# Kernel optimization log

Hardware: AMD Instinct MI355X
Metric: run time of the kernel (lower is better)

Reference implementation:

```python
import jax, jax.numpy as jnp
import numpy as np

HIDDEN = 1024
HEADS = 16
HEAD_DIM = 64
B, S = 2, 2048
SCALE = 1.0 / np.sqrt(HEAD_DIM)
NEG = -1e9


def setup_inputs() -> dict:
    key = jax.random.key(0)
    k1, k2, k3, k4, k5 = jax.random.split(key, 5)
    hidden_states = jax.random.normal(k1, (B, S, HIDDEN), dtype=jnp.float32)
    # causal additive mask, broadcast over heads: [B, 1, S, S]
    causal = jnp.where(jnp.tril(jnp.ones((S, S), dtype=bool)), 0.0, NEG).astype(jnp.float32)
    attention_mask = jnp.broadcast_to(causal[None, None], (B, 1, S, S))
    std = 1.0 / np.sqrt(HIDDEN)
    Wq = jax.random.normal(k2, (HIDDEN, HEADS * HEAD_DIM), dtype=jnp.float32) * std
    Wk = jax.random.normal(k3, (HIDDEN, HEADS * HEAD_DIM), dtype=jnp.float32) * std
    Wv = jax.random.normal(k4, (HIDDEN, HEADS * HEAD_DIM), dtype=jnp.float32) * std
    Wo = jax.random.normal(k5, (HEADS * HEAD_DIM, HIDDEN), dtype=jnp.float32) * std
    return {"hidden_states": hidden_states, "attention_mask": attention_mask,
            "Wq": Wq, "Wk": Wk, "Wv": Wv, "Wo": Wo}


def reference(hidden_states, attention_mask, Wq, Wk, Wv, Wo):
    b, s, _ = hidden_states.shape
    # projections (eval mode: dropouts are identity)
    q = (hidden_states @ Wq).reshape(b, s, HEADS, HEAD_DIM).transpose(0, 2, 1, 3)  # [B,H,S,D]
    k = (hidden_states @ Wk).reshape(b, s, HEADS, HEAD_DIM).transpose(0, 2, 1, 3)
    v = (hidden_states @ Wv).reshape(b, s, HEADS, HEAD_DIM).transpose(0, 2, 1, 3)
    scores = jnp.einsum('bhqd,bhkd->bhqk', q, k) * SCALE + attention_mask  # [B,H,S,S]
    probs = jax.nn.softmax(scores, axis=-1)
    out = jnp.einsum('bhqk,bhkd->bhqd', probs, v)  # [B,H,S,D]
    out = out.transpose(0, 2, 1, 3).reshape(b, s, HEADS * HEAD_DIM)
    return out @ Wo  # [B,S,HIDDEN]
```

## Files before the change

### kernel.cpp

```cpp
#include <hip/hip_runtime.h>

typedef unsigned short u16;
typedef unsigned int u32;
typedef __bf16 bf16x8 __attribute__((ext_vector_type(8)));
typedef float f32x4 __attribute__((ext_vector_type(4)));

#define MFMA(a, b, c) __builtin_amdgcn_mfma_f32_16x16x32_bf16(a, b, c, 0, 0, 0)

#define GLD16(gsrc, ldst)                                                          \
  __builtin_amdgcn_global_load_lds(                                                \
      (const __attribute__((address_space(1))) void*)(gsrc),                       \
      (__attribute__((address_space(3))) void*)(ldst), 16, 0, 0)

#if __has_builtin(__builtin_amdgcn_exp2f)
#define EXP2(x) __builtin_amdgcn_exp2f(x)
#else
#define EXP2(x) exp2f(x)
#endif

__device__ __forceinline__ u16 f2bf(float f) {
  return __builtin_bit_cast(u16, (__bf16)f);
}

__device__ __forceinline__ u32 pk2(float a, float b) {
  __bf16 x = (__bf16)a, y = (__bf16)b;
  return (u32)__builtin_bit_cast(u16, x) | ((u32)__builtin_bit_cast(u16, y) << 16);
}

__device__ __forceinline__ float bf2f(u16 u) {
  return __builtin_bit_cast(float, ((u32)u) << 16);
}

__global__ __launch_bounds__(256) void k_prep(
    const float* __restrict__ X, const float* __restrict__ Wq,
    const float* __restrict__ Wk, const float* __restrict__ Wv,
    const float* __restrict__ Wo, u16* __restrict__ Xb,
    u16* __restrict__ Wt, u16* __restrict__ Wot) {
  __shared__ u16 t[32][33];
  int bid = blockIdx.x;
  if (bid < 2048) {
    int i = bid * 256 + threadIdx.x;
    const float4* p = (const float4*)X + (size_t)i * 2;
    float4 a = p[0], b = p[1];
    uint4 o;
    o.x = pk2(a.x, a.y);
    o.y = pk2(a.z, a.w);
    o.z = pk2(b.x, b.y);
    o.w = pk2(b.z, b.w);
    *(uint4*)(Xb + (size_t)i * 8) = o;
    return;
  }
  bid -= 2048;
  const int k0 = (bid & 31) * 32, n0 = (bid >> 5) * 32;
  const int x = threadIdx.x & 31, y = threadIdx.x >> 5;
  const float* src = (n0 < 1024) ? Wq : (n0 < 2048) ? Wk : (n0 < 3072) ? Wv : Wo;
  const int ncol = n0 & 1023;
#pragma unroll
  for (int rr = 0; rr < 4; ++rr) {
    int kl = y + rr * 8;
    t[x][kl] = f2bf(src[(size_t)(k0 + kl) * 1024 + ncol + x]);
  }
  __syncthreads();
  u16* dst = (n0 < 3072) ? (Wt + (size_t)n0 * 1024) : (Wot + (size_t)(n0 - 3072) * 1024);
#pragma unroll
  for (int rr = 0; rr < 4; ++rr) {
    int nl = y + rr * 8;
    dst[(size_t)nl * 1024 + k0 + x] = t[nl][x];
  }
}


__global__ __launch_bounds__(256) void k_gemm_qkv(const u16* __restrict__ A_,
                                                  const u16* __restrict__ Bt,
                                                  u16* __restrict__ Q,
                                                  u16* __restrict__ K,
                                                  u16* __restrict__ Vt) {
  __shared__ __align__(16) u16 As[2][128 * 32];
  __shared__ __align__(16) u16 Bs[2][64 * 32];
  const int tid = threadIdx.x;
  const int w = tid >> 6, l = tid & 63;
  const int lr = l & 15, lg = l >> 4;
  const int lin = blockIdx.y * 48 + blockIdx.x;
  const int swz = (lin & 7) * 192 + (lin >> 3);
  const int tM = (swz / 48) * 128, tN = (swz % 48) * 64;
  const int bufsel = tN >> 10;

  const int srow = l >> 2;
  const int scol = (((l & 3) ^ ((l >> 3) & 3)) << 3);
  const u16* Ag = A_ + (size_t)(tM + srow) * 1024 + scol;
  const u16* Bg = Bt + (size_t)(tN + srow) * 1024 + scol;
  const int rs = (lr >> 1) & 3;

#define STAGE_QKV(buf, kk)                                                   \
  {                                                                          \
    GLD16(Ag + (size_t)(w * 16) * 1024 + (kk), &As[buf][(w * 16) * 32]);     \
    GLD16(Ag + (size_t)(64 + w * 16) * 1024 + (kk), &As[buf][(64 + w * 16) * 32]); \
    GLD16(Bg + (size_t)(w * 16) * 1024 + (kk), &Bs[buf][(w * 16) * 32]);     \
  }

  f32x4 acc[2][4] = {};
  STAGE_QKV(0, 0)
  __syncthreads();
  int cur = 0;

  if (bufsel < 2) {
    for (int t = 0; t < 32; ++t) {
      if (t < 31) STAGE_QKV(cur ^ 1, (t + 1) * 32)
      const u16* Ac = &As[cur][0];
      const u16* Bc = &Bs[cur][0];
      bf16x8 a[2], b[4];
#pragma unroll
      for (int m = 0; m < 2; ++m)
        a[m] = *(const bf16x8*)(Ac + (w * 32 + m * 16 + lr) * 32 + ((lg ^ rs) << 3));
#pragma unroll
      for (int n = 0; n < 4; ++n)
        b[n] = *(const bf16x8*)(Bc + (n * 16 + lr) * 32 + ((lg ^ rs) << 3));
#pragma unroll
      for (int m = 0; m < 2; ++m)
#pragma unroll
        for (int n = 0; n < 4; ++n) acc[m][n] = MFMA(b[n], a[m], acc[m][n]);
      __syncthreads();
      cur ^= 1;
    }
    u16* dst = bufsel ? K : Q;
    const float sc = bufsel ? 1.0f : 0.180336880111124f;
#pragma unroll
    for (int m = 0; m < 2; ++m) {
      int s = tM + w * 32 + m * 16 + lr;
      int b_ = s >> 11, sr2 = s & 2047;
#pragma unroll
      for (int n = 0; n < 4; ++n) {
        int c2 = (tN + n * 16 + lg * 4) & 1023;
        int h = c2 >> 6, d = c2 & 63;
        uint2 val;
        val.x = pk2(acc[m][n][0] * sc, acc[m][n][1] * sc);
        val.y = pk2(acc[m][n][2] * sc, acc[m][n][3] * sc);
        *(uint2*)(dst + ((size_t)(b_ * 16 + h) * 2048 + sr2) * 64 + d) = val;
      }
    }
  } else {
    for (int t = 0; t < 32; ++t) {
      if (t < 31) STAGE_QKV(cur ^ 1, (t + 1) * 32)
      const u16* Ac = &As[cur][0];
      const u16* Bc = &Bs[cur][0];
      bf16x8 a[2], b[4];
#pragma unroll
      for (int m = 0; m < 2; ++m)
        a[m] = *(const bf16x8*)(Ac + (w * 32 + m * 16 + lr) * 32 + ((lg ^ rs) << 3));
#pragma unroll
      for (int n = 0; n < 4; ++n)
        b[n] = *(const bf16x8*)(Bc + (n * 16 + lr) * 32 + ((lg ^ rs) << 3));
#pragma unroll
      for (int m = 0; m < 2; ++m)
#pragma unroll
        for (int n = 0; n < 4; ++n) acc[m][n] = MFMA(a[m], b[n], acc[m][n]);
      __syncthreads();
      cur ^= 1;
    }
#pragma unroll
    for (int m = 0; m < 2; ++m) {
      int r0 = tM + w * 32 + m * 16 + lg * 4;
      int b_ = r0 >> 11, s0 = r0 & 2047;
#pragma unroll
      for (int n = 0; n < 4; ++n) {
        int c2 = (tN + n * 16 + lr) & 1023;
        int h = c2 >> 6, d = c2 & 63;
        uint2 val;
        val.x = pk2(acc[m][n][0], acc[m][n][1]);
        val.y = pk2(acc[m][n][2], acc[m][n][3]);
        *(uint2*)(Vt + ((size_t)(b_ * 16 + h) * 64 + d) * 2048 + s0) = val;
      }
    }
  }
#undef STAGE_QKV
}

__global__ __launch_bounds__(256, 4) void k_attn(const u16* __restrict__ Q,
                                                 const u16* __restrict__ Kg,
                                                 const u16* __restrict__ Vtg,
                                                 u16* __restrict__ AO,
                                                 u16* __restrict__ PO,
                                                 float* __restrict__ ML) {
  __shared__ __align__(16) u16 Ks[2][64 * 64];
  __shared__ __align__(16) u16 Vs[2][64 * 64];
  __shared__ __align__(16) u16 Ps[4][16 * 64];
  const int tid = threadIdx.x;
  const int w = tid >> 6, l = tid & 63;
  const int lr = l & 15, lg = l >> 4;

  const int idx = blockIdx.x;
  const int bh = idx & 31;
  const int g = idx >> 5;
  int qt, c0;
  if (g < 16) { qt = 16 + g; c0 = 0; }
  else if (g < 32) { qt = 31 - (g - 16); c0 = 1; }
  else { qt = 15 - (g - 32); c0 = 0; }
  const int nkt = (qt < 16) ? (qt + 1) : (c0 == 0 ? 16 : qt - 15);
  const bool hasdiag = (qt < 16) || (c0 == 1);
  const int q0 = qt * 64;

  const u16* Qp = Q + (size_t)bh * 2048 * 64;
  const u16* Kp = Kg + (size_t)bh * 2048 * 64;
  const u16* Vp = Vtg + (size_t)bh * 64 * 2048;

  const int qrow = q0 + w * 16 + lr;
  bf16x8 qa0 = *(const bf16x8*)(Qp + (size_t)qrow * 64 + lg * 8);
  bf16x8 qa1 = *(const bf16x8*)(Qp + (size_t)qrow * 64 + 32 + lg * 8);

  f32x4 oacc[4] = {};
  float m_run = -1e30f, l_run = 0.f;

  const int srow = l >> 3;
  const int scol = ((l & 7) ^ srow) * 8;
  const int sw = (lr & 7) << 3;

  const u16* kptr = Kp + ((size_t)c0 * 1024 + srow) * 64 + scol;
  const u16* vptr = Vp + (size_t)srow * 2048 + c0 * 1024 + scol;

#pragma unroll
  for (int j = 0; j < 2; ++j) {
    int base = j * 32 + w * 8;
    GLD16(kptr + base * 64, &Ks[0][base * 64]);
    GLD16(vptr + (size_t)base * 2048, &Vs[0][base * 64]);
  }
  kptr += 4096;
  vptr += 64;
  __syncthreads();

  int cur = 0;

#define ATTN_TILE(DOPRE, DOMASK)                                                   \
  {                                                                                \
    if (DOPRE) {                                                                   \
      _Pragma("unroll") for (int j = 0; j < 2; ++j) {                              \
        int base = j * 32 + w * 8;                                                 \
        GLD16(kptr + base * 64, &Ks[cur ^ 1][base * 64]);                          \
        GLD16(vptr + (size_t)base * 2048, &Vs[cur ^ 1][base * 64]);                \
      }                                                                            \
      kptr += 4096;                                                                \
      vptr += 64;                                                                  \
    }                                                                              \
    f32x4 st[4];                                                                   \
    _Pragma("unroll") for (int n = 0; n < 4; ++n) {                                \
      const u16* kr = &Ks[cur][(n * 16 + lr) * 64];                                \
      bf16x8 kb0 = *(const bf16x8*)(kr + ((lg << 3) ^ sw));                        \
      bf16x8 kb1 = *(const bf16x8*)(kr + (((4 + lg) << 3) ^ sw));                  \
      f32x4 z = {0.f, 0.f, 0.f, 0.f};                                              \
      z = MFMA(kb0, qa0, z);                                                       \
      z = MFMA(kb1, qa1, z);                                                       \
      st[n] = z;                                                                   \
    }                                                                              \
    float mx = -1e30f;                                                             \
    _Pragma("unroll") for (int n = 0; n < 4; ++n)                                  \
        _Pragma("unroll") for (int j = 0; j < 4; ++j) {                            \
      float s = st[n][j];                                                          \
      if (DOMASK && (n * 16 + lg * 4 + j) > (w * 16 + lr)) s = -1e30f;             \
      st[n][j] = s;                                                                \
      mx = fmaxf(mx, s);                                                           \
    }                                                                              \
    mx = fmaxf(mx, __shfl_xor(mx, 16, 64));                                        \
    mx = fmaxf(mx, __shfl_xor(mx, 32, 64));                                        \
    const bool grow = __any(mx > m_run);                                           \
    float mnew = grow ? fmaxf(m_run, mx) : m_run;                                  \
    float rsum = 0.f;                                                              \
    _Pragma("unroll") for (int n = 0; n < 4; ++n)                                  \
        _Pragma("unroll") for (int j = 0; j < 4; ++j) {                            \
      float p = EXP2(st[n][j] - mnew);                                             \
      st[n][j] = p;                                                                \
      rsum += p;                                                                   \
    }                                                                              \
    rsum += __shfl_xor(rsum, 16, 64);                                              \
    rsum += __shfl_xor(rsum, 32, 64);                                              \
    if (grow) {                                                                    \
      float fsc = EXP2(m_run - mnew);                                              \
      l_run = l_run * fsc + rsum;                                                  \
      m_run = mnew;                                                                \
      _Pragma("unroll") for (int n = 0; n < 4; ++n)                                \
          _Pragma("unroll") for (int j = 0; j < 4; ++j) oacc[n][j] *= fsc;         \
    } else {                                                                       \
      l_run += rsum;                                                               \
    }                                                                              \
    u16* pb = &Ps[w][0];                                                           \
    _Pragma("unroll") for (int n = 0; n < 4; ++n) {                                \
      int slot = n * 2 + (lg >> 1);                                                \
      int off = lr * 64 + ((slot ^ (lr & 7)) << 3) + (lg & 1) * 4;                 \
      uint2 val;                                                                   \
      val.x = pk2(st[n][0], st[n][1]);                                             \
      val.y = pk2(st[n][2], st[n][3]);                                             \
      *(uint2*)(pb + off) = val;                                                   \
    }                                                                              \
    bf16x8 pa0 = *(const bf16x8*)(pb + lr * 64 + ((lg << 3) ^ sw));                \
    bf16x8 pa1 = *(const bf16x8*)(pb + lr * 64 + (((4 + lg) << 3) ^ sw));          \
    _Pragma("unroll") for (int n = 0; n < 4; ++n) {                                \
      const u16* vr = &Vs[cur][(n * 16 + lr) * 64];                                \
      bf16x8 vb0 = *(const bf16x8*)(vr + ((lg << 3) ^ sw));                        \
      bf16x8 vb1 = *(const bf16x8*)(vr + (((4 + lg) << 3) ^ sw));                  \
      oacc[n] = MFMA(vb0, pa0, oacc[n]);                                           \
      oacc[n] = MFMA(vb1, pa1, oacc[n]);                                           \
    }                                                                              \
  }

  for (int it = 0; it < nkt - 1; ++it) {
    ATTN_TILE(true, false);
    __syncthreads();
    cur ^= 1;
  }
  if (hasdiag) {
    ATTN_TILE(false, true);
  } else {
    ATTN_TILE(false, false);
  }
#undef ATTN_TILE

  if (qt < 16) {
    const int b_ = bh >> 4, h = bh & 15;
    const float linv = 1.0f / l_run;
    const int s = q0 + w * 16 + lr;
    u16* dst = AO + ((size_t)(b_ * 2048 + s)) * 1024 + h * 64 + lg * 4;
#pragma unroll
    for (int n = 0; n < 4; ++n) {
      uint2 val;
      val.x = pk2(oacc[n][0] * linv, oacc[n][1] * linv);
      val.y = pk2(oacc[n][2] * linv, oacc[n][3] * linv);
      *(uint2*)(dst + n * 16) = val;
    }
  } else {
    const int p = (bh * 16 + (qt - 16)) * 2 + c0;
    u16* po = PO + (size_t)p * 4096 + (size_t)(w * 16 + lr) * 64 + lg * 4;
#pragma unroll
    for (int n = 0; n < 4; ++n) {
      uint2 val;
      val.x = pk2(oacc[n][0], oacc[n][1]);
      val.y = pk2(oacc[n][2], oacc[n][3]);
      *(uint2*)(po + n * 16) = val;
    }
    if (lg == 0) {
      ML[(size_t)p * 128 + (w * 16 + lr)] = m_run;
      ML[(size_t)p * 128 + 64 + (w * 16 + lr)] = l_run;
    }
  }
}

__global__ __launch_bounds__(256) void k_combine(const u16* __restrict__ PO,
                                                 const float* __restrict__ ML,
                                                 u16* __restrict__ AO) {
  const int blk = blockIdx.x;
  const int bh = blk >> 4, qt = 16 + (blk & 15);
  const int row = threadIdx.x >> 2;
  const int dseg = (threadIdx.x & 3) * 16;
  const size_t p0 = (size_t)blk * 2;
  const float m0 = ML[p0 * 128 + row], l0 = ML[p0 * 128 + 64 + row];
  const float m1 = ML[p0 * 128 + 128 + row], l1 = ML[p0 * 128 + 192 + row];
  const float M = fmaxf(m0, m1);
  float w0 = EXP2(m0 - M), w1 = EXP2(m1 - M);
  const float inv = 1.0f / (l0 * w0 + l1 * w1);
  w0 *= inv;
  w1 *= inv;
  const u16* o0 = PO + p0 * 4096 + (size_t)row * 64 + dseg;
  const u16* o1 = o0 + 4096;
  const int b_ = bh >> 4, h = bh & 15;
  u16* dst = AO + ((size_t)(b_ * 2048 + qt * 64 + row)) * 1024 + h * 64 + dseg;
#pragma unroll
  for (int half = 0; half < 2; ++half) {
    uint4 a = *(const uint4*)(o0 + half * 8);
    uint4 b = *(const uint4*)(o1 + half * 8);
    u32 aw[4] = {a.x, a.y, a.z, a.w};
    u32 bw[4] = {b.x, b.y, b.z, b.w};
    uint4 o;
    u32 ow[4];
#pragma unroll
    for (int i = 0; i < 4; ++i) {
      float r0 = bf2f((u16)(aw[i] & 0xffffu)) * w0 + bf2f((u16)(bw[i] & 0xffffu)) * w1;
      float r1 = bf2f((u16)(aw[i] >> 16)) * w0 + bf2f((u16)(bw[i] >> 16)) * w1;
      ow[i] = pk2(r0, r1);
    }
    o.x = ow[0]; o.y = ow[1]; o.z = ow[2]; o.w = ow[3];
    *(uint4*)(dst + half * 8) = o;
  }
}

__global__ __launch_bounds__(256) void k_gemm_out(const u16* __restrict__ A_,
                                                  const u16* __restrict__ Bt,
                                                  float* __restrict__ out) {
  __shared__ __align__(16) u16 As[2][128 * 32];
  __shared__ __align__(16) u16 Bs[2][64 * 32];
  const int tid = threadIdx.x;
  const int w = tid >> 6, l = tid & 63;
  const int lr = l & 15, lg = l >> 4;
  const int lin = blockIdx.y * 16 + blockIdx.x;
  const int swz = (lin & 7) * 64 + (lin >> 3);
  const int tM = (swz / 16) * 128, tN = (swz % 16) * 64;

  const int srow = l >> 2;
  const int scol = (((l & 3) ^ ((l >> 3) & 3)) << 3);
  const u16* Ag = A_ + (size_t)(tM + srow) * 1024 + scol;
  const u16* Bg = Bt + (size_t)(tN + srow) * 1024 + scol;
  const int rs = (lr >> 1) & 3;

#define STAGE_OUT(buf, kk)                                                   \
  {                                                                          \
    GLD16(Ag + (size_t)(w * 16) * 1024 + (kk), &As[buf][(w * 16) * 32]);     \
    GLD16(Ag + (size_t)(64 + w * 16) * 1024 + (kk), &As[buf][(64 + w * 16) * 32]); \
    GLD16(Bg + (size_t)(w * 16) * 1024 + (kk), &Bs[buf][(w * 16) * 32]);     \
  }

  f32x4 acc[2][4] = {};
  STAGE_OUT(0, 0)
  __syncthreads();
  int cur = 0;
  for (int t = 0; t < 32; ++t) {
    if (t < 31) STAGE_OUT(cur ^ 1, (t + 1) * 32)
    const u16* Ac = &As[cur][0];
    const u16* Bc = &Bs[cur][0];
    bf16x8 a[2], b[4];
#pragma unroll
    for (int m = 0; m < 2; ++m)
      a[m] = *(const bf16x8*)(Ac + (w * 32 + m * 16 + lr) * 32 + ((lg ^ rs) << 3));
#pragma unroll
    for (int n = 0; n < 4; ++n)
      b[n] = *(const bf16x8*)(Bc + (n * 16 + lr) * 32 + ((lg ^ rs) << 3));
#pragma unroll
    for (int m = 0; m < 2; ++m)
#pragma unroll
      for (int n = 0; n < 4; ++n) acc[m][n] = MFMA(b[n], a[m], acc[m][n]);
    __syncthreads();
    cur ^= 1;
  }
#undef STAGE_OUT

#pragma unroll
  for (int m = 0; m < 2; ++m) {
    int s = tM + w * 32 + m * 16 + lr;
#pragma unroll
    for (int n = 0; n < 4; ++n) {
      int c = tN + n * 16 + lg * 4;
      float4 v;
      v.x = acc[m][n][0];
      v.y = acc[m][n][1];
      v.z = acc[m][n][2];
      v.w = acc[m][n][3];
      *(float4*)(out + (size_t)s * 1024 + c) = v;
    }
  }
}

extern "C" void kernel_launch(void* const* d_in, const int* in_sizes, int n_in,
                              void* d_out, int out_size, void* d_ws, size_t ws_size,
                              hipStream_t stream) {
  const float* X = (const float*)d_in[0];
  const float* Wq = (const float*)d_in[2];
  const float* Wk = (const float*)d_in[3];
  const float* Wv = (const float*)d_in[4];
  const float* Wo = (const float*)d_in[5];
  float* out = (float*)d_out;

  char* ws = (char*)d_ws;
  if (ws_size < (size_t)48 * 1024 * 1024) return;
  u16* Xb  = (u16*)(ws);
  u16* Wt  = (u16*)(ws + 8388608);
  u16* Wot = (u16*)(ws + 14680064);
  u16* Q   = (u16*)(ws + 16777216);
  u16* K   = (u16*)(ws + 25165824);
  u16* Vt  = (u16*)(ws + 33554432);
  u16* AO  = (u16*)(ws + 41943040);
  u16*   PO = (u16*)(ws);
  float* ML = (float*)(ws + 8388608);

  k_prep<<<6144, 256, 0, stream>>>(X, Wq, Wk, Wv, Wo, Xb, Wt, Wot);
  k_gemm_qkv<<<dim3(48, 32), 256, 0, stream>>>(Xb, Wt, Q, K, Vt);
  k_attn<<<1536, 256, 0, stream>>>(Q, K, Vt, AO, PO, ML);
  k_combine<<<512, 256, 0, stream>>>(PO, ML, AO);
  k_gemm_out<<<dim3(16, 32), 256, 0, stream>>>(AO, Wot, out);
}
```

Before: 128.3 us.

## Triple-buffer GEMM staging with vmcnt waits and enlarge QKV tile to 128x128

```diff
diff --git a/kernel.cpp b/kernel.cpp
--- a/kernel.cpp
+++ b/kernel.cpp
@@ -17,6 +17,13 @@
 #else
 #define EXP2(x) exp2f(x)
 #endif
+
+#define WAITBAR(N)                                                                 \
+  {                                                                                \
+    asm volatile("s_waitcnt vmcnt(" #N ")" ::: "memory");                          \
+    __builtin_amdgcn_s_barrier();                                                  \
+    __builtin_amdgcn_sched_barrier(0);                                             \
+  }
 
 __device__ __forceinline__ u16 f2bf(float f) {
   return __builtin_bit_cast(u16, (__bf16)f);
@@ -75,14 +82,15 @@
                                                   u16* __restrict__ Q,
                                                   u16* __restrict__ K,
                                                   u16* __restrict__ Vt) {
-  __shared__ __align__(16) u16 As[2][128 * 32];
-  __shared__ __align__(16) u16 Bs[2][64 * 32];
+  __shared__ __align__(16) u16 As[3 * 128 * 32];
+  __shared__ __align__(16) u16 Bs[3 * 128 * 32];
   const int tid = threadIdx.x;
   const int w = tid >> 6, l = tid & 63;
   const int lr = l & 15, lg = l >> 4;
-  const int lin = blockIdx.y * 48 + blockIdx.x;
-  const int swz = (lin & 7) * 192 + (lin >> 3);
-  const int tM = (swz / 48) * 128, tN = (swz % 48) * 64;
+  const int lin = blockIdx.y * 24 + blockIdx.x;
+  const int swz = (lin & 7) * 96 + (lin >> 3);
+  const int tM = (swz / 24) * 128, tN = (swz % 24) * 128;
+  const int wr = w >> 1, wc = w & 1;
   const int bufsel = tN >> 10;
 
   const int srow = l >> 2;
@@ -91,46 +99,73 @@
   const u16* Bg = Bt + (size_t)(tN + srow) * 1024 + scol;
   const int rs = (lr >> 1) & 3;
 
-#define STAGE_QKV(buf, kk)                                                   \
-  {                                                                          \
-    GLD16(Ag + (size_t)(w * 16) * 1024 + (kk), &As[buf][(w * 16) * 32]);     \
-    GLD16(Ag + (size_t)(64 + w * 16) * 1024 + (kk), &As[buf][(64 + w * 16) * 32]); \
-    GLD16(Bg + (size_t)(w * 16) * 1024 + (kk), &Bs[buf][(w * 16) * 32]);     \
-  }
-
-  f32x4 acc[2][4] = {};
+#define STAGE_QKV(buf, kk)                                                         \
+  {                                                                                \
+    GLD16(Ag + (size_t)(w * 16) * 1024 + (kk), As + (buf) * 4096 + (w * 16) * 32); \
+    GLD16(Ag + (size_t)(64 + w * 16) * 1024 + (kk),                                \
+          As + (buf) * 4096 + (64 + w * 16) * 32);                                 \
+    GLD16(Bg + (size_t)(w * 16) * 1024 + (kk), Bs + (buf) * 4096 + (w * 16) * 32); \
+    GLD16(Bg + (size_t)(64 + w * 16) * 1024 + (kk),                                \
+          Bs + (buf) * 4096 + (64 + w * 16) * 32);                                 \
+  }
+
+#define QKV_FRAGS(buf)                                                             \
+  const u16* Ac = As + (buf) * 4096;                                               \
+  const u16* Bc = Bs + (buf) * 4096;                                               \
+  bf16x8 a[4], b[4];                                                               \
+  _Pragma("unroll") for (int m = 0; m < 4; ++m)                                    \
+      a[m] = *(const bf16x8*)(Ac + (wr * 64 + m * 16 + lr) * 32 +                  \
+                              ((lg ^ rs) << 3));                                   \
+  _Pragma("unroll") for (int n = 0; n < 4; ++n)                                    \
+      b[n] = *(const bf16x8*)(Bc + (wc * 64 + n * 16 + lr) * 32 +                  \
+                              ((lg ^ rs) << 3));
+
+#define QKV_MFMA_SWAP                                                              \
+  _Pragma("unroll") for (int m = 0; m < 4; ++m)                                    \
+      _Pragma("unroll") for (int n = 0; n < 4; ++n)                                \
+          acc[m][n] = MFMA(b[n], a[m], acc[m][n]);
+
+#define QKV_MFMA_NORM                                                              \
+  _Pragma("unroll") for (int m = 0; m < 4; ++m)                                    \
+      _Pragma("unroll") for (int n = 0; n < 4; ++n)                                \
+          acc[m][n] = MFMA(a[m], b[n], acc[m][n]);
+
+  f32x4 acc[4][4] = {};
   STAGE_QKV(0, 0)
-  __syncthreads();
-  int cur = 0;
+  STAGE_QKV(1, 32)
+  WAITBAR(4)
+  int cur = 0, nxt = 2;
 
   if (bufsel < 2) {
-    for (int t = 0; t < 32; ++t) {
-      if (t < 31) STAGE_QKV(cur ^ 1, (t + 1) * 32)
-      const u16* Ac = &As[cur][0];
-      const u16* Bc = &Bs[cur][0];
-      bf16x8 a[2], b[4];
-#pragma unroll
-      for (int m = 0; m < 2; ++m)
-        a[m] = *(const bf16x8*)(Ac + (w * 32 + m * 16 + lr) * 32 + ((lg ^ rs) << 3));
-#pragma unroll
-      for (int n = 0; n < 4; ++n)
-        b[n] = *(const bf16x8*)(Bc + (n * 16 + lr) * 32 + ((lg ^ rs) << 3));
-#pragma unroll
-      for (int m = 0; m < 2; ++m)
-#pragma unroll
-        for (int n = 0; n < 4; ++n) acc[m][n] = MFMA(b[n], a[m], acc[m][n]);
-      __syncthreads();
-      cur ^= 1;
+    for (int t = 0; t < 30; ++t) {
+      STAGE_QKV(nxt, (t + 2) * 32)
+      {
+        QKV_FRAGS(cur)
+        QKV_MFMA_SWAP
+      }
+      WAITBAR(4)
+      cur = (cur == 2) ? 0 : cur + 1;
+      nxt = (nxt == 2) ? 0 : nxt + 1;
+    }
+    {
+      QKV_FRAGS(cur)
+      QKV_MFMA_SWAP
+    }
+    WAITBAR(0)
+    cur = (cur == 2) ? 0 : cur + 1;
+    {
+      QKV_FRAGS(cur)
+      QKV_MFMA_SWAP
     }
     u16* dst = bufsel ? K : Q;
     const float sc = bufsel ? 1.0f : 0.180336880111124f;
 #pragma unroll
-    for (int m = 0; m < 2; ++m) {
-      int s = tM + w * 32 + m * 16 + lr;
+    for (int m = 0; m < 4; ++m) {
+      int s = tM + wr * 64 + m * 16 + lr;
       int b_ = s >> 11, sr2 = s & 2047;
 #pragma unroll
       for (int n = 0; n < 4; ++n) {
-        int c2 = (tN + n * 16 + lg * 4) & 1023;
+        int c2 = (tN + wc * 64 + n * 16 + lg * 4) & 1023;
         int h = c2 >> 6, d = c2 & 63;
         uint2 val;
         val.x = pk2(acc[m][n][0] * sc, acc[m][n][1] * sc);
@@ -139,31 +174,33 @@
       }
     }
   } else {
-    for (int t = 0; t < 32; ++t) {
-      if (t < 31) STAGE_QKV(cur ^ 1, (t + 1) * 32)
-      const u16* Ac = &As[cur][0];
-      const u16* Bc = &Bs[cur][0];
-      bf16x8 a[2], b[4];
-#pragma unroll
-      for (int m = 0; m < 2; ++m)
-        a[m] = *(const bf16x8*)(Ac + (w * 32 + m * 16 + lr) * 32 + ((lg ^ rs) << 3));
-#pragma unroll
-      for (int n = 0; n < 4; ++n)
-        b[n] = *(const bf16x8*)(Bc + (n * 16 + lr) * 32 + ((lg ^ rs) << 3));
-#pragma unroll
-      for (int m = 0; m < 2; ++m)
-#pragma unroll
-        for (int n = 0; n < 4; ++n) acc[m][n] = MFMA(a[m], b[n], acc[m][n]);
-      __syncthreads();
-      cur ^= 1;
-    }
-#pragma unroll
-    for (int m = 0; m < 2; ++m) {
-      int r0 = tM + w * 32 + m * 16 + lg * 4;
+    for (int t = 0; t < 30; ++t) {
+      STAGE_QKV(nxt, (t + 2) * 32)
+      {
+        QKV_FRAGS(cur)
+        QKV_MFMA_NORM
+      }
+      WAITBAR(4)
+      cur = (cur == 2) ? 0 : cur + 1;
+      nxt = (nxt == 2) ? 0 : nxt + 1;
+    }
+    {
+      QKV_FRAGS(cur)
+      QKV_MFMA_NORM
+    }
+    WAITBAR(0)
+    cur = (cur == 2) ? 0 : cur + 1;
+    {
+      QKV_FRAGS(cur)
+      QKV_MFMA_NORM
+    }
+#pragma unroll
+    for (int m = 0; m < 4; ++m) {
+      int r0 = tM + wr * 64 + m * 16 + lg * 4;
       int b_ = r0 >> 11, s0 = r0 & 2047;
 #pragma unroll
       for (int n = 0; n < 4; ++n) {
-        int c2 = (tN + n * 16 + lr) & 1023;
+        int c2 = (tN + wc * 64 + n * 16 + lr) & 1023;
         int h = c2 >> 6, d = c2 & 63;
         uint2 val;
         val.x = pk2(acc[m][n][0], acc[m][n][1]);
@@ -173,6 +210,9 @@
     }
   }
 #undef STAGE_QKV
+#undef QKV_FRAGS
+#undef QKV_MFMA_SWAP
+#undef QKV_MFMA_NORM
 }
 
 __global__ __launch_bounds__(256, 4) void k_attn(const u16* __restrict__ Q,
@@ -382,8 +422,8 @@
 __global__ __launch_bounds__(256) void k_gemm_out(const u16* __restrict__ A_,
                                                   const u16* __restrict__ Bt,
                                                   float* __restrict__ out) {
-  __shared__ __align__(16) u16 As[2][128 * 32];
-  __shared__ __align__(16) u16 Bs[2][64 * 32];
+  __shared__ __align__(16) u16 As[3 * 128 * 32];
+  __shared__ __align__(16) u16 Bs[3 * 64 * 32];
   const int tid = threadIdx.x;
   const int w = tid >> 6, l = tid & 63;
   const int lr = l & 15, lg = l >> 4;
@@ -397,36 +437,47 @@
   const u16* Bg = Bt + (size_t)(tN + srow) * 1024 + scol;
   const int rs = (lr >> 1) & 3;
 
-#define STAGE_OUT(buf, kk)                                                   \
-  {                                                                          \
-    GLD16(Ag + (size_t)(w * 16) * 1024 + (kk), &As[buf][(w * 16) * 32]);     \
-    GLD16(Ag + (size_t)(64 + w * 16) * 1024 + (kk), &As[buf][(64 + w * 16) * 32]); \
-    GLD16(Bg + (size_t)(w * 16) * 1024 + (kk), &Bs[buf][(w * 16) * 32]);     \
+#define STAGE_OUT(buf, kk)                                                         \
+  {                                                                                \
+    GLD16(Ag + (size_t)(w * 16) * 1024 + (kk), As + (buf) * 4096 + (w * 16) * 32); \
+    GLD16(Ag + (size_t)(64 + w * 16) * 1024 + (kk),                                \
+          As + (buf) * 4096 + (64 + w * 16) * 32);                                 \
+    GLD16(Bg + (size_t)(w * 16) * 1024 + (kk), Bs + (buf) * 2048 + (w * 16) * 32); \
+  }
+
+#define OUT_COMPUTE(buf)                                                           \
+  {                                                                                \
+    const u16* Ac = As + (buf) * 4096;                                             \
+    const u16* Bc = Bs + (buf) * 2048;                                             \
+    bf16x8 a[2], b[4];                                                             \
+    _Pragma("unroll") for (int m = 0; m < 2; ++m)                                  \
+        a[m] = *(const bf16x8*)(Ac + (w * 32 + m * 16 + lr) * 32 +                 \
+                                ((lg ^ rs) << 3));                                 \
+    _Pragma("unroll") for (int n = 0; n < 4; ++n)                                  \
+        b[n] = *(const bf16x8*)(Bc + (n * 16 + lr) * 32 + ((lg ^ rs) << 3));       \
+    _Pragma("unroll") for (int m = 0; m < 2; ++m)                                  \
+        _Pragma("unroll") for (int n = 0; n < 4; ++n)                              \
+            acc[m][n] = MFMA(b[n], a[m], acc[m][n]);                               \
   }
 
   f32x4 acc[2][4] = {};
   STAGE_OUT(0, 0)
-  __syncthreads();
-  int cur = 0;
-  for (int t = 0; t < 32; ++t) {
-    if (t < 31) STAGE_OUT(cur ^ 1, (t + 1) * 32)
-    const u16* Ac = &As[cur][0];
-    const u16* Bc = &Bs[cur][0];
-    bf16x8 a[2], b[4];
-#pragma unroll
-    for (int m = 0; m < 2; ++m)
-      a[m] = *(const bf16x8*)(Ac + (w * 32 + m * 16 + lr) * 32 + ((lg ^ rs) << 3));
-#pragma unroll
-    for (int n = 0; n < 4; ++n)
-      b[n] = *(const bf16x8*)(Bc + (n * 16 + lr) * 32 + ((lg ^ rs) << 3));
-#pragma unroll
-    for (int m = 0; m < 2; ++m)
-#pragma unroll
-      for (int n = 0; n < 4; ++n) acc[m][n] = MFMA(b[n], a[m], acc[m][n]);
-    __syncthreads();
-    cur ^= 1;
-  }
+  STAGE_OUT(1, 32)
+  WAITBAR(3)
+  int cur = 0, nxt = 2;
+  for (int t = 0; t < 30; ++t) {
+    STAGE_OUT(nxt, (t + 2) * 32)
+    OUT_COMPUTE(cur)
+    WAITBAR(3)
+    cur = (cur == 2) ? 0 : cur + 1;
+    nxt = (nxt == 2) ? 0 : nxt + 1;
+  }
+  OUT_COMPUTE(cur)
+  WAITBAR(0)
+  cur = (cur == 2) ? 0 : cur + 1;
+  OUT_COMPUTE(cur)
 #undef STAGE_OUT
+#undef OUT_COMPUTE
 
 #pragma unroll
   for (int m = 0; m < 2; ++m) {
@@ -467,7 +518,7 @@
   float* ML = (float*)(ws + 8388608);
 
   k_prep<<<6144, 256, 0, stream>>>(X, Wq, Wk, Wv, Wo, Xb, Wt, Wot);
-  k_gemm_qkv<<<dim3(48, 32), 256, 0, stream>>>(Xb, Wt, Q, K, Vt);
+  k_gemm_qkv<<<dim3(24, 32), 256, 0, stream>>>(Xb, Wt, Q, K, Vt);
   k_attn<<<1536, 256, 0, stream>>>(Q, K, Vt, AO, PO, ML);
   k_combine<<<512, 256, 0, stream>>>(PO, ML, AO);
   k_gemm_out<<<dim3(16, 32), 256, 0, stream>>>(AO, Wot, out);
```

After: 125.9 us. Within noise of the previous version (-1.9%).
